# Kernel tuning notes

Measured on AMD Instinct MI355X. Metric: run time of the kernel, lower is better.

Reference implementation:

```python
import jax, jax.numpy as jnp
import numpy as np

N_QUBITS = 8          # == hidden_dim
DIM = 2 ** N_QUBITS   # statevector size
EMBED = 512
VOCAB = 50257
SEQ = 128
BATCH = 256


def _cnot_chain_perm(n):
    # CNOT(w,w+1) for w in 0..n-2, then CNOT(n-1,0); wire 0 = MSB.
    f = np.arange(2 ** n)
    pairs = [(w, w + 1) for w in range(n - 1)] + [(n - 1, 0)]
    for c, t in pairs:
        cbit = (f >> (n - 1 - c)) & 1
        f = f ^ (cbit << (n - 1 - t))
    inv = np.empty_like(f)
    inv[f] = np.arange(2 ** n)
    return inv

_PERM_INV = jnp.asarray(_cnot_chain_perm(N_QUBITS))
# signs[j, k] = <j|Z_k|j> = 1 - 2*bit_k(j), wire 0 = MSB
_j = np.arange(DIM)[:, None]
_SIGNS = jnp.asarray(1.0 - 2.0 * ((_j >> (N_QUBITS - 1 - np.arange(N_QUBITS))) & 1), dtype=jnp.float32)


def qlayer(y, theta):
    """RX(y_i) encoder + trainable RX(theta_i) (same axis -> RX(y+theta)),
    CNOT ring, PauliZ expectation per wire.  y: (B, n) -> (B, n)."""
    half = 0.5 * (y + theta)
    c = jnp.cos(half).astype(jnp.complex64)
    s = (-1j) * jnp.sin(half).astype(jnp.complex64)
    B = y.shape[0]
    state = jnp.ones((B, 1), jnp.complex64)
    for w in range(N_QUBITS):  # fixed small structural loop (kron build)
        amp = jnp.stack([c[:, w], s[:, w]], axis=1)  # (B, 2)
        state = (state[:, :, None] * amp[:, None, :]).reshape(B, -1)
    state = state[:, _PERM_INV]                       # apply CNOT ring
    probs = jnp.real(state * jnp.conj(state))         # (B, 2^n)
    return probs @ _SIGNS                             # (B, n)


def setup_inputs() -> dict:
    key = jax.random.key(0)
    ks = jax.random.split(key, 16)
    d_in = EMBED + N_QUBITS
    inp = {
        "sentence": jax.random.randint(ks[0], (SEQ, BATCH), 0, VOCAB),
        "features": jax.random.normal(ks[1], (BATCH, N_QUBITS), jnp.float32),
        "emb_table": 0.02 * jax.random.normal(ks[2], (VOCAB, EMBED), jnp.float32),
        "W_f": 0.05 * jax.random.normal(ks[3], (N_QUBITS, d_in), jnp.float32),
        "b_f": jnp.zeros((N_QUBITS,), jnp.float32),
        "W_i": 0.05 * jax.random.normal(ks[4], (N_QUBITS, d_in), jnp.float32),
        "b_i": jnp.zeros((N_QUBITS,), jnp.float32),
        "W_u": 0.05 * jax.random.normal(ks[5], (N_QUBITS, d_in), jnp.float32),
        "b_u": jnp.zeros((N_QUBITS,), jnp.float32),
        "W_o": 0.05 * jax.random.normal(ks[6], (N_QUBITS, d_in), jnp.float32),
        "b_o": jnp.zeros((N_QUBITS,), jnp.float32),
        "th_f": jax.random.normal(ks[7], (N_QUBITS,), jnp.float32),
        "th_i": jax.random.normal(ks[8], (N_QUBITS,), jnp.float32),
        "th_u": jax.random.normal(ks[9], (N_QUBITS,), jnp.float32),
        "th_o": jax.random.normal(ks[10], (N_QUBITS,), jnp.float32),
    }
    return inp


def reference(sentence, features, emb_table, W_f, b_f, W_i, b_i, W_u, b_u,
              W_o, b_o, th_f, th_i, th_u, th_o):
    embeds = emb_table[sentence]               # (T, B, E)
    B = embeds.shape[1]
    h0 = jnp.zeros((B, N_QUBITS), jnp.float32)
    c0 = jnp.zeros((B, N_QUBITS), jnp.float32)

    def step(carry, xt):
        hx, cx = carry
        comb = jnp.concatenate([xt, hx], axis=1)          # (B, E+H)
        f = jax.nn.sigmoid(qlayer(comb @ W_f.T + b_f, th_f))
        i = jax.nn.sigmoid(qlayer(comb @ W_i.T + b_i, th_i))
        g = jnp.tanh(qlayer(comb @ W_u.T + b_u, th_u))
        o = jax.nn.sigmoid(qlayer(comb @ W_o.T + b_o, th_o))
        cx = f * cx + i * g
        hx = o * jnp.tanh(cx)
        return (hx, cx), hx

    (hx, cx), outs = jax.lax.scan(step, (h0, c0), embeds)
    cls_input = outs[-1]                        # lstm_out[-1]: (B, H)
    return cls_input
```

## Files before the change

kernel.cpp:

```cpp
#include <hip/hip_runtime.h>
#include <hip/hip_bf16.h>

#define NQ     8
#define SEQL   128
#define BATCHN 256
#define EMBED  512
#define DIN    520
#define GSTR   32
#define GBSTR  40
#define INV2PI 0.15915494309189535f
#define WROW   524

typedef __attribute__((ext_vector_type(8))) short  bf16x8;
typedef __attribute__((ext_vector_type(4))) float  f32x4;
typedef unsigned int uint2v __attribute__((ext_vector_type(2)));

__device__ __forceinline__ bf16x8 cvt8(float4 u, float4 v) {
    union { unsigned w[4]; bf16x8 v8; } r;
    asm("v_cvt_pk_bf16_f32 %0, %1, %2" : "=v"(r.w[0]) : "v"(u.x), "v"(u.y));
    asm("v_cvt_pk_bf16_f32 %0, %1, %2" : "=v"(r.w[1]) : "v"(u.z), "v"(u.w));
    asm("v_cvt_pk_bf16_f32 %0, %1, %2" : "=v"(r.w[2]) : "v"(v.x), "v"(v.y));
    asm("v_cvt_pk_bf16_f32 %0, %1, %2" : "=v"(r.w[3]) : "v"(v.z), "v"(v.w));
    return r.v8;
}

#define DPP_QP(a,b,c,d) ((a)|((b)<<2)|((c)<<4)|((d)<<6))
#define DPP_SHL(n) (0x100+(n))
#define DPP_SHR(n) (0x110+(n))
#define DPP_ROR(n) (0x120+(n))

template<int CTRL>
__device__ __forceinline__ float updpf(float old_, float src) {
    return __int_as_float(__builtin_amdgcn_update_dpp(
        __float_as_int(old_), __float_as_int(src), CTRL, 0xF, 0xF, false));
}

__device__ __forceinline__ float xor16f(float x) {
    unsigned xu = (unsigned)__float_as_int(x);
    uint2v r = __builtin_amdgcn_permlane16_swap(xu, xu, false, false);
    return __int_as_float((int)(r.x ^ r.y ^ xu));
}

__device__ __forceinline__ float frcp(float x) { return __builtin_amdgcn_rcpf(x); }
__device__ __forceinline__ float fexp2(float x) { return __builtin_amdgcn_exp2f(x); }

#define LOG2E  1.4426950408889634f
#define LOG2E2 2.8853900817779268f

#define QSTEP(GV) do {                                                        \
    float sA = fmaf(H[0],Whp[0],fmaf(H[1],Whp[1],fmaf(H[2],Whp[2],H[3]*Whp[3]))); \
    float sB = fmaf(H[4],Whp[4],fmaf(H[5],Whp[5],fmaf(H[6],Whp[6],H[7]*Whp[7]))); \
    float cs = __builtin_amdgcn_cosf((GV) + sA + sB);                         \
    float p = cs, s;                                                          \
    s = updpf<DPP_SHR(1)>(1.0f, p); p *= (m1 ? s : 1.0f);                     \
    s = updpf<DPP_SHR(2)>(1.0f, p); p *= (m2 ? s : 1.0f);                     \
    s = updpf<DPP_SHR(4)>(1.0f, p); p *= (m4 ? s : 1.0f);                     \
    float v = jz ? 1.0f : cs;                                                 \
    v *= updpf<DPP_QP(1,0,3,2)>(v, v);                                        \
    v *= updpf<DPP_QP(2,3,0,1)>(v, v);                                        \
    float xl = updpf<DPP_SHL(4)>(v, v);                                       \
    float xr = updpf<DPP_SHR(4)>(v, v);                                       \
    v *= (m4 ? xr : xl);                                                      \
    float qv = jz ? v : p;                                                    \
    float act = fmaf(sk, frcp(1.0f + fexp2(ek * qv)), ok);                    \
    float A_  = act;                                                          \
    float B8  = updpf<DPP_ROR(8)>(A_, A_);                                    \
    float C16 = xor16f(A_);                                                   \
    float D24 = updpf<DPP_ROR(8)>(C16, C16);                                  \
    float fv = (g==0) ? A_ : (g==1) ? B8 : (g==2) ? C16 : D24;                \
    float iv = (g==1) ? A_ : (g==0) ? B8 : (g==3) ? C16 : D24;                \
    float uv = (g==2) ? A_ : (g==3) ? B8 : (g==0) ? C16 : D24;                \
    float ov = (g==3) ? A_ : (g==2) ? B8 : (g==1) ? C16 : D24;                \
    c_own = fmaf(fv, c_own, iv * uv);                                         \
    float tc = fmaf(-2.0f, frcp(1.0f + fexp2(LOG2E2 * c_own)), 1.0f);         \
    h_own = ov * tc;                                                          \
    H[0] = h_own;                                                             \
    H[1] = updpf<DPP_QP(1,0,3,2)>(H[0], H[0]);                                \
    H[2] = updpf<DPP_QP(2,3,0,1)>(H[0], H[0]);                                \
    H[3] = updpf<DPP_QP(2,3,0,1)>(H[1], H[1]);                                \
    _Pragma("unroll")                                                         \
    for (int rr = 0; rr < 4; ++rr) {                                          \
        float yl = updpf<DPP_SHL(4)>(H[rr], H[rr]);                           \
        float yr = updpf<DPP_SHR(4)>(H[rr], H[rr]);                           \
        H[4 + rr] = m4 ? yr : yl;                                             \
    }                                                                         \
} while (0)

#define PRODUCE(DST, CH) do {                                                 \
    int tok_ = sent[((CH) * 16 + lm) * BATCHN + b];                           \
    const float* ar_ = emb + (size_t)tok_ * EMBED;                            \
    float4 ua[16], va[16];                                                    \
    _Pragma("unroll")                                                         \
    for (int kc = 0; kc < 16; ++kc) {                                         \
        ua[kc] = *reinterpret_cast<const float4*>(ar_ + kc * 32 + q * 8);     \
        va[kc] = *reinterpret_cast<const float4*>(ar_ + kc * 32 + q * 8 + 4); \
    }                                                                         \
    f32x4 acc0 = {0.f,0.f,0.f,0.f};                                           \
    f32x4 acc1 = {0.f,0.f,0.f,0.f};                                           \
    _Pragma("unroll")                                                         \
    for (int kc = 0; kc < 16; ++kc) {                                         \
        bf16x8 a_ = cvt8(ua[kc], va[kc]);                                     \
        const int kl_ = kc * 32 + q * 8;                                      \
        bf16x8 b0_ = *reinterpret_cast<const bf16x8*>(&Wlds[lm][kl_]);        \
        bf16x8 b1_ = *reinterpret_cast<const bf16x8*>(&Wlds[16 + lm][kl_]);   \
        acc0 = __builtin_amdgcn_mfma_f32_16x16x32_bf16(a_, b0_, acc0, 0,0,0); \
        acc1 = __builtin_amdgcn_mfma_f32_16x16x32_bf16(a_, b1_, acc1, 0,0,0); \
    }                                                                         \
    _Pragma("unroll")                                                         \
    for (int r_ = 0; r_ < 4; ++r_) {                                          \
        (DST)[(4*q + r_) * GBSTR + lm]      = fmaf(acc0[r_], INV2PI, bc0);    \
        (DST)[(4*q + r_) * GBSTR + 16 + lm] = fmaf(acc1[r_], INV2PI, bc1);    \
    }                                                                         \
} while (0)

__global__ __launch_bounds__(128, 1)
void k_fused(const int* __restrict__ sent, const float* __restrict__ emb,
             const float* __restrict__ Wf, const float* __restrict__ Wi,
             const float* __restrict__ Wu, const float* __restrict__ Wo,
             const float* __restrict__ bf, const float* __restrict__ bi,
             const float* __restrict__ bu, const float* __restrict__ bo,
             const float* __restrict__ thf, const float* __restrict__ thi,
             const float* __restrict__ thu, const float* __restrict__ tho,
             float* __restrict__ out)
{
    __shared__ short Wlds[32][WROW];
    __shared__ float gbuf[2][16 * GBSTR];

    const int tid = threadIdx.x;
    const int b   = blockIdx.x;
    const bool producer = (tid >= 64);
    const int l32 = tid & 31;
    const int g   = l32 >> 3;
    const int j   = l32 & 7;
    const int lm  = tid & 15;
    const int q   = (tid >> 4) & 3;

    {
        const int c = tid & 31, seg = tid >> 5;
        const int gg = c >> 3, jj = c & 7;
        const float* W = (gg==0) ? Wf : (gg==1) ? Wi : (gg==2) ? Wu : Wo;
        const float* src = W + (size_t)jj * DIN + seg * 128;
        #pragma unroll
        for (int p = 0; p < 16; ++p) {
            float4 u = *reinterpret_cast<const float4*>(src + p * 8);
            float4 v = *reinterpret_cast<const float4*>(src + p * 8 + 4);
            *reinterpret_cast<bf16x8*>(&Wlds[c][seg * 128 + p * 8]) = cvt8(u, v);
        }
    }

    float Whp[8], H[8];
    float c_own = 0.f, h_own = 0.f;
    float bc0 = 0.f, bc1 = 0.f;
    bool  m1 = false, m2 = false, m4 = false, jz = false;
    float ek = 0.f, sk = 0.f, ok = 0.f;

    if (producer) {
        const int g0 = lm >> 3, j0 = lm & 7;
        const float* B0 = (g0==0) ? bf  : bi;
        const float* T0 = (g0==0) ? thf : thi;
        bc0 = (B0[j0] + T0[j0]) * INV2PI;
        const float* B1 = (g0==0) ? bu  : bo;
        const float* T1 = (g0==0) ? thu : tho;
        bc1 = (B1[j0] + T1[j0]) * INV2PI;
    } else {
        const float* Wsel = (g==0) ? Wf : (g==1) ? Wi : (g==2) ? Wu : Wo;
        #pragma unroll
        for (int rr = 0; rr < 8; ++rr) {
            Whp[rr] = Wsel[j * DIN + EMBED + (j ^ rr)] * INV2PI;
            H[rr]   = 0.f;
        }
        m1 = (j >= 1); m2 = (j >= 2); m4 = (j >= 4); jz = (j == 0);
        const bool isU = (g == 2);
        ek = isU ? LOG2E2 : -LOG2E;
        sk = isU ? -2.0f  : 1.0f;
        ok = isU ? 1.0f   : 0.0f;
    }
    __syncthreads();

    if (producer) PRODUCE(&gbuf[0][0], 0);
    __syncthreads();

    #pragma unroll 1
    for (int c = 0; c < 8; ++c) {
        if (producer) {
            if (c < 7) PRODUCE(&gbuf[(c + 1) & 1][0], c + 1);
        } else {
            const float* gc = &gbuf[c & 1][l32];
            float gvv[16];
            #pragma unroll
            for (int s = 0; s < 16; ++s) gvv[s] = gc[s * GBSTR];
            #pragma unroll
            for (int s = 0; s < 16; ++s) QSTEP(gvv[s]);
        }
        __syncthreads();
    }

    if (tid < 8) out[b * NQ + tid] = h_own;
}

extern "C" void kernel_launch(void* const* d_in, const int* in_sizes, int n_in,
                              void* d_out, int out_size, void* d_ws, size_t ws_size,
                              hipStream_t stream)
{
    const int*   sent = (const int*)  d_in[0];
    const float* emb  = (const float*)d_in[2];
    const float* Wf   = (const float*)d_in[3];
    const float* bf   = (const float*)d_in[4];
    const float* Wi   = (const float*)d_in[5];
    const float* bi   = (const float*)d_in[6];
    const float* Wu   = (const float*)d_in[7];
    const float* bu   = (const float*)d_in[8];
    const float* Wo   = (const float*)d_in[9];
    const float* bo   = (const float*)d_in[10];
    const float* thf  = (const float*)d_in[11];
    const float* thi  = (const float*)d_in[12];
    const float* thu  = (const float*)d_in[13];
    const float* tho  = (const float*)d_in[14];
    float* out = (float*)d_out;

    k_fused<<<BATCHN, 128, 0, stream>>>(sent, emb, Wf, Wi, Wu, Wo,
                                        bf, bi, bu, bo,
                                        thf, thi, thu, tho, out);
}
```

Measured before the change: 36.00 us.

## Prefetch first embedding chunk before weight staging and shorten recurrent critical path

The producer warps now issue the global loads for the first token chunk's embedding rows before the weight-to-LDS staging, so that load latency overlaps the setup phase. The first chunk's MFMA projection is then done inline from the prefetched registers. Separately, the per-step recurrent dot product is rebalanced into a shallower FMA tree that folds in the input gate value early. The hidden-state broadcast now builds H[3] and H[5..7] directly from H[0] and H[4], which shortens the serial DPP chain. The cost is higher register pressure in the producer warps from holding 32 float4 values across the staging code.

```diff
diff --git a/kernel.cpp b/kernel.cpp
--- a/kernel.cpp
+++ b/kernel.cpp
@@ -48,9 +48,12 @@
 #define LOG2E2 2.8853900817779268f
 
 #define QSTEP(GV) do {                                                        \
-    float sA = fmaf(H[0],Whp[0],fmaf(H[1],Whp[1],fmaf(H[2],Whp[2],H[3]*Whp[3]))); \
-    float sB = fmaf(H[4],Whp[4],fmaf(H[5],Whp[5],fmaf(H[6],Whp[6],H[7]*Whp[7]))); \
-    float cs = __builtin_amdgcn_cosf((GV) + sA + sB);                         \
+    float t0 = fmaf(H[1], Whp[1], (GV));                                      \
+    t0 = fmaf(H[0], Whp[0], t0);                                              \
+    float t1 = fmaf(H[2], Whp[2], H[3] * Whp[3]);                             \
+    float t2 = fmaf(H[4], Whp[4], H[5] * Whp[5]);                             \
+    float t3 = fmaf(H[6], Whp[6], H[7] * Whp[7]);                             \
+    float cs = __builtin_amdgcn_cosf((t0 + t1) + (t2 + t3));                  \
     float p = cs, s;                                                          \
     s = updpf<DPP_SHR(1)>(1.0f, p); p *= (m1 ? s : 1.0f);                     \
     s = updpf<DPP_SHR(2)>(1.0f, p); p *= (m2 ? s : 1.0f);                     \
@@ -77,13 +80,13 @@
     H[0] = h_own;                                                             \
     H[1] = updpf<DPP_QP(1,0,3,2)>(H[0], H[0]);                                \
     H[2] = updpf<DPP_QP(2,3,0,1)>(H[0], H[0]);                                \
-    H[3] = updpf<DPP_QP(2,3,0,1)>(H[1], H[1]);                                \
-    _Pragma("unroll")                                                         \
-    for (int rr = 0; rr < 4; ++rr) {                                          \
-        float yl = updpf<DPP_SHL(4)>(H[rr], H[rr]);                           \
-        float yr = updpf<DPP_SHR(4)>(H[rr], H[rr]);                           \
-        H[4 + rr] = m4 ? yr : yl;                                             \
-    }                                                                         \
+    H[3] = updpf<DPP_QP(3,2,1,0)>(H[0], H[0]);                                \
+    float yl4 = updpf<DPP_SHL(4)>(H[0], H[0]);                                \
+    float yr4 = updpf<DPP_SHR(4)>(H[0], H[0]);                                \
+    H[4] = m4 ? yr4 : yl4;                                                    \
+    H[5] = updpf<DPP_QP(1,0,3,2)>(H[4], H[4]);                                \
+    H[6] = updpf<DPP_QP(2,3,0,1)>(H[4], H[4]);                                \
+    H[7] = updpf<DPP_QP(3,2,1,0)>(H[4], H[4]);                                \
 } while (0)
 
 #define PRODUCE(DST, CH) do {                                                 \
@@ -135,6 +138,17 @@
     const int lm  = tid & 15;
     const int q   = (tid >> 4) & 3;
 
+    float4 pua[16], pva[16];
+    if (producer) {
+        int tok0 = sent[lm * BATCHN + b];
+        const float* ar = emb + (size_t)tok0 * EMBED;
+        #pragma unroll
+        for (int kc = 0; kc < 16; ++kc) {
+            pua[kc] = *reinterpret_cast<const float4*>(ar + kc * 32 + q * 8);
+            pva[kc] = *reinterpret_cast<const float4*>(ar + kc * 32 + q * 8 + 4);
+        }
+    }
+
     {
         const int c = tid & 31, seg = tid >> 5;
         const int gg = c >> 3, jj = c & 7;
@@ -177,7 +191,24 @@
     }
     __syncthreads();
 
-    if (producer) PRODUCE(&gbuf[0][0], 0);
+    if (producer) {
+        f32x4 acc0 = {0.f,0.f,0.f,0.f};
+        f32x4 acc1 = {0.f,0.f,0.f,0.f};
+        #pragma unroll
+        for (int kc = 0; kc < 16; ++kc) {
+            bf16x8 a_ = cvt8(pua[kc], pva[kc]);
+            const int kl_ = kc * 32 + q * 8;
+            bf16x8 b0_ = *reinterpret_cast<const bf16x8*>(&Wlds[lm][kl_]);
+            bf16x8 b1_ = *reinterpret_cast<const bf16x8*>(&Wlds[16 + lm][kl_]);
+            acc0 = __builtin_amdgcn_mfma_f32_16x16x32_bf16(a_, b0_, acc0, 0,0,0);
+            acc1 = __builtin_amdgcn_mfma_f32_16x16x32_bf16(a_, b1_, acc1, 0,0,0);
+        }
+        #pragma unroll
+        for (int r_ = 0; r_ < 4; ++r_) {
+            gbuf[0][(4*q + r_) * GBSTR + lm]      = fmaf(acc0[r_], INV2PI, bc0);
+            gbuf[0][(4*q + r_) * GBSTR + 16 + lm] = fmaf(acc1[r_], INV2PI, bc1);
+        }
+    }
     __syncthreads();
 
     #pragma unroll 1
```

Measured after the change: 38.45 us. 6.8% more time.
